# Kernel optimization log

Hardware: AMD Instinct MI355X
Metric: run time of the kernel (lower is better)

The kernel has to match this reference:

```python
import jax, jax.numpy as jnp
import numpy as np

DIM = 192
HEADS = 6
WIN = (8, 7, 7)
SHIFT = (4, 3, 3)


def _rel_pos_index(ws):
    coords = np.stack(np.meshgrid(np.arange(ws[0]), np.arange(ws[1]), np.arange(ws[2]), indexing='ij'))
    cf = coords.reshape(3, -1)
    rc = (cf[:, :, None] - cf[:, None, :]).transpose(1, 2, 0).copy()
    rc[:, :, 0] += ws[0] - 1
    rc[:, :, 1] += ws[1] - 1
    rc[:, :, 2] += ws[2] - 1
    rc[:, :, 0] *= (2 * ws[1] - 1) * (2 * ws[2] - 1)
    rc[:, :, 1] *= 2 * ws[2] - 1
    return rc.sum(-1)  # [N, N]


def _attn_mask(size_dhw, ws, ss):
    # static (shape-only) shift mask, [num_windows, N, N]
    D, H, W = size_dhw
    m = np.zeros(size_dhw, dtype=np.float32)
    sl = [((0, -ws[i]), (-ws[i], -ss[i]), (-ss[i], None)) for i in range(3)]
    cnt = 0
    for d in sl[0]:
        for h in sl[1]:
            for w in sl[2]:
                m[d[0]:d[1], h[0]:h[1], w[0]:w[1]] = cnt
                cnt += 1
    nW = (D // ws[0]) * (H // ws[1]) * (W // ws[2])
    m = m.reshape(D // ws[0], ws[0], H // ws[1], ws[1], W // ws[2], ws[2])
    m = m.transpose(0, 2, 4, 1, 3, 5).reshape(nW, -1)
    diff = m[:, None, :] - m[:, :, None]  # unsqueeze(1) - unsqueeze(2)
    return np.where(diff != 0, np.float32(-100.0), np.float32(0.0))


def setup_inputs() -> dict:
    key = jax.random.key(0)
    ks = jax.random.split(key, 6)
    c = DIM
    x = jax.random.normal(ks[0], (1, 16, 56, 56, c), dtype=jnp.float32)
    qkv_weight = jax.random.normal(ks[1], (3 * c, c), dtype=jnp.float32) * 0.02
    qkv_bias = jax.random.normal(ks[2], (3 * c,), dtype=jnp.float32) * 0.02
    proj_weight = jax.random.normal(ks[3], (c, c), dtype=jnp.float32) * 0.02
    proj_bias = jax.random.normal(ks[4], (c,), dtype=jnp.float32) * 0.02
    tbl = (2 * WIN[0] - 1) * (2 * WIN[1] - 1) * (2 * WIN[2] - 1)
    rel_bias_table = jax.random.normal(ks[5], (tbl, HEADS), dtype=jnp.float32) * 0.02
    return {'x': x, 'qkv_weight': qkv_weight, 'qkv_bias': qkv_bias,
            'proj_weight': proj_weight, 'proj_bias': proj_bias,
            'rel_bias_table': rel_bias_table}


def _forward(x, qkv_weight, qkv_bias, proj_weight, proj_bias, rel_bias_table):
    b, d, h, w, c = x.shape
    ws = list(WIN)
    ss = list(SHIFT)
    for i, s in enumerate((d, h, w)):
        if s <= ws[i]:
            ws[i] = s
            ss[i] = 0
    N = ws[0] * ws[1] * ws[2]
    # relative position bias [1, heads, N, N]
    idx = _rel_pos_index(ws)[:N, :N].reshape(-1)
    rpb = rel_bias_table[idx].reshape(N, N, HEADS).transpose(2, 0, 1)[None]
    # pad to multiples of window
    pad = [(ws[i] - (d, h, w)[i] % ws[i]) % ws[i] for i in range(3)]
    xp = jnp.pad(x, ((0, 0), (0, pad[0]), (0, pad[1]), (0, pad[2]), (0, 0)))
    dp, hp, wp = d + pad[0], h + pad[1], w + pad[2]
    shifted = sum(ss) > 0
    if shifted:
        xp = jnp.roll(xp, shift=(-ss[0], -ss[1], -ss[2]), axis=(1, 2, 3))
    nW = (dp // ws[0]) * (hp // ws[1]) * (wp // ws[2])
    # window partition -> [b*nW, N, c]
    xw = xp.reshape(b, dp // ws[0], ws[0], hp // ws[1], ws[1], wp // ws[2], ws[2], c)
    xw = xw.transpose(0, 1, 3, 5, 2, 4, 6, 7).reshape(b * nW, N, c)
    hd = c // HEADS
    qkv = xw @ qkv_weight.T + qkv_bias
    qkv = qkv.reshape(b * nW, N, 3, HEADS, hd).transpose(2, 0, 3, 1, 4)
    q, k, v = qkv[0], qkv[1], qkv[2]  # [b*nW, heads, N, hd]
    q = q * (hd ** -0.5)
    attn = jnp.einsum('whnd,whmd->whnm', q, k) + rpb
    if shifted:
        mask = jnp.asarray(_attn_mask((dp, hp, wp), ws, ss))  # [nW, N, N]
        attn = attn.reshape(b, nW, HEADS, N, N) + mask[None, :, None]
        attn = attn.reshape(b * nW, HEADS, N, N)
    attn = jax.nn.softmax(attn, axis=-1)
    out = jnp.einsum('whnm,whmd->whnd', attn, v)
    out = out.transpose(0, 2, 1, 3).reshape(b * nW, N, c)
    out = out @ proj_weight.T + proj_bias
    # window reverse
    out = out.reshape(b, dp // ws[0], hp // ws[1], wp // ws[2], ws[0], ws[1], ws[2], c)
    out = out.transpose(0, 1, 4, 2, 5, 3, 6, 7).reshape(b, dp, hp, wp, c)
    if shifted:
        out = jnp.roll(out, shift=(ss[0], ss[1], ss[2]), axis=(1, 2, 3))
    return out[:, :d, :h, :w, :]


def reference(x, qkv_weight, qkv_bias, proj_weight, proj_bias, rel_bias_table):
    return _forward(x, qkv_weight, qkv_bias, proj_weight, proj_bias, rel_bias_table)
```

## Files before the change

kernel.cpp:

```cpp
#include <hip/hip_runtime.h>


typedef _Float16 f16;
typedef __attribute__((ext_vector_type(8))) _Float16 f16x8;
typedef __attribute__((ext_vector_type(4))) _Float16 f16x4;
typedef __attribute__((ext_vector_type(4))) float f32x4;

#define MFMA16(a, b, c) __builtin_amdgcn_mfma_f32_16x16x32_f16((a), (b), (c), 0, 0, 0)

#define HEADS 6
#define NWIN 128
#define NTOK 392
#define TOKENS (NWIN * NTOK)
#define CDIM 192

__device__ inline f16x8 f16x8_zero() {
    f16x8 v = {(f16)0.f,(f16)0.f,(f16)0.f,(f16)0.f,(f16)0.f,(f16)0.f,(f16)0.f,(f16)0.f};
    return v;
}

__global__ __launch_bounds__(256) void wconv_kernel(
    const float* __restrict__ wqkv, const float* __restrict__ wproj,
    f16* __restrict__ wqkv_h, f16* __restrict__ wproj_h)
{
    int i = blockIdx.x * 256 + threadIdx.x;
    if (i < 576 * 192) wqkv_h[i] = (f16)wqkv[i];
    if (i < 192 * 192) wproj_h[i] = (f16)wproj[i];
}

__global__ __launch_bounds__(256) void rpb_kernel(
    const float* __restrict__ tbl, float* __restrict__ rpb)
{
    int i = blockIdx.x * 256 + threadIdx.x;
    if (i >= 6 * 400 * 400) return;
    int h = i / 160000;
    int r = i - h * 160000;
    int n = r / 400;
    int m = r - n * 400;
    float v;
    if (n < NTOK && m < NTOK) {
        int td = n / 49, t2 = n - td * 49, th = t2 / 7, tw = t2 - th * 7;
        int md = m / 49, m2 = m - md * 49, mh = m2 / 7, mw = m2 - mh * 7;
        int idx = ((td - md + 7) * 13 + (th - mh + 6)) * 13 + (tw - mw + 6);
        v = tbl[idx * 6 + h];
    } else {
        v = -1e30f;
    }
    rpb[i] = v;
}

__global__ __launch_bounds__(256, 2) void qkv_kernel(
    const float* __restrict__ x, const f16* __restrict__ wq,
    const float* __restrict__ bq,
    f16* __restrict__ q_ws, f16* __restrict__ k_ws, f16* __restrict__ v_ws)
{
    __shared__ __align__(16) f16 a_lds[64 * 256];
    const int tid = threadIdx.x;
    const int bm = blockIdx.x * 64;
    const int bn = blockIdx.y * 192;

    for (int i = tid; i < 64 * 24; i += 256) {
        int row = i / 24, c = i - row * 24;
        int tok = bm + row;
        int win = tok / NTOK, nloc = tok - win * NTOK;
        int td = nloc / 49, r2 = nloc - td * 49, th = r2 / 7, tw = r2 - th * 7;
        int wd = win >> 6, wh = (win >> 3) & 7, ww = win & 7;
        int d = (wd * 8 + td + 4) & 15;
        int hh = wh * 7 + th + 3; if (hh >= 56) hh -= 56;
        int wco = ww * 7 + tw + 3; if (wco >= 56) wco -= 56;
        const float* src = x + ((d * 56 + hh) * 56 + wco) * CDIM + c * 8;
        const float4 u0 = *(const float4*)(src);
        const float4 u1 = *(const float4*)(src + 4);
        f16x8 v;
        v[0] = (f16)u0.x; v[1] = (f16)u0.y; v[2] = (f16)u0.z; v[3] = (f16)u0.w;
        v[4] = (f16)u1.x; v[5] = (f16)u1.y; v[6] = (f16)u1.z; v[7] = (f16)u1.w;
        *(f16x8*)&a_lds[row * 256 + ((c ^ (row & 7)) << 3)] = v;
    }
    __syncthreads();

    const int lane = tid & 63, wv = tid >> 6;
    const int l15 = lane & 15, g = lane >> 4;
    const int m0 = (wv & 1) * 32, n0 = (wv >> 1) * 96;

    const f32x4 z4 = {0.f, 0.f, 0.f, 0.f};
    f32x4 acc[2][6];
    #pragma unroll
    for (int mi = 0; mi < 2; mi++)
        #pragma unroll
        for (int ni = 0; ni < 6; ni++) acc[mi][ni] = z4;

    #pragma unroll
    for (int kk = 0; kk < 6; kk++) {
        f16x8 af[2];
        #pragma unroll
        for (int mi = 0; mi < 2; mi++) {
            int row = m0 + mi * 16 + l15;
            af[mi] = *(const f16x8*)&a_lds[row * 256 + (((kk * 4 + g) ^ (row & 7)) << 3)];
        }
        #pragma unroll
        for (int ni = 0; ni < 6; ni++) {
            const f16x8 bf = *(const f16x8*)&wq[(bn + n0 + ni * 16 + l15) * CDIM + kk * 32 + g * 8];
            #pragma unroll
            for (int mi = 0; mi < 2; mi++)
                acc[mi][ni] = MFMA16(af[mi], bf, acc[mi][ni]);
        }
    }

    #pragma unroll
    for (int mi = 0; mi < 2; mi++) {
        const int tok0 = bm + m0 + mi * 16 + g * 4;
        const int win = tok0 / NTOK, nloc0 = tok0 - win * NTOK;
        #pragma unroll
        for (int ni = 0; ni < 6; ni++) {
            const int n = bn + n0 + ni * 16 + l15;
            const float bias = bq[n];
            if (bn == 0) {
                const int head = n >> 5, hd = n & 31;
                f16* dst = q_ws + ((win * HEADS + head) * NTOK + nloc0) * 32 + hd;
                #pragma unroll
                for (int j = 0; j < 4; j++)
                    dst[j * 32] = (f16)((acc[mi][ni][j] + bias) * 0.17677669529663687f);
            } else if (bn == 192) {
                const int cc = n - 192, head = cc >> 5, hd = cc & 31;
                f16* dst = k_ws + ((win * HEADS + head) * NTOK + nloc0) * 32 + hd;
                #pragma unroll
                for (int j = 0; j < 4; j++)
                    dst[j * 32] = (f16)(acc[mi][ni][j] + bias);
            } else {
                const int cc = n - 384, head = cc >> 5, hd = cc & 31;
                f16x4 pk;
                #pragma unroll
                for (int j = 0; j < 4; j++) pk[j] = (f16)(acc[mi][ni][j] + bias);
                *(f16x4*)(v_ws + ((win * HEADS + head) * 32 + hd) * NTOK + nloc0) = pk;
            }
        }
    }
}

__global__ __launch_bounds__(256, 2) void attn_kernel(
    const f16* __restrict__ q_ws, const f16* __restrict__ k_ws,
    const f16* __restrict__ v_ws, const float* __restrict__ rpb,
    f16* __restrict__ o_ws)
{
    __shared__ __align__(16) f16 k_lds[25 * 512];
    __shared__ __align__(16) f16 v_lds[13 * 1024];
    __shared__ __align__(16) f16 p_scr[4][512];
    __shared__ unsigned char region[400];

    const int tid = threadIdx.x;
    const int bid = blockIdx.x;
    const int win = bid / 6, head = bid - win * 6;
    const int wd = win >> 6, wh = (win >> 3) & 7, ww = win & 7;
    const f16* kb = k_ws + (win * HEADS + head) * NTOK * 32;
    const f16* vb = v_ws + (win * HEADS + head) * 32 * NTOK;
    const f16* qb = q_ws + (win * HEADS + head) * NTOK * 32;

    for (int i = tid; i < 400; i += 256) {
        unsigned char rr = 0;
        if (i < NTOK) {
            int td = i / 49, r2 = i - td * 49, th = r2 / 7, tw = r2 - th * 7;
            int rd = (wd == 1) ? (td < 4 ? 1 : 2) : 0;
            int rh = (wh == 7) ? (th < 4 ? 1 : 2) : 0;
            int rw = (ww == 7) ? (tw < 4 ? 1 : 2) : 0;
            rr = (unsigned char)(rd * 9 + rh * 3 + rw);
        }
        region[i] = rr;
    }
    for (int i = tid; i < 1600; i += 256) {
        const int tok = ((i >> 6) << 4) | (i & 15);
        const int gg = (i >> 4) & 3;
        f16x8 v = f16x8_zero();
        if (tok < NTOK) v = *(const f16x8*)(kb + tok * 32 + gg * 8);
        *(f16x8*)&k_lds[i * 8] = v;
    }
    for (int i = tid; i < 1664; i += 256) {
        const int tb = i >> 7, rest = i & 127;
        const int hd = ((rest >> 6) << 4) | (rest & 15);
        const int gg = (rest >> 4) & 3;
        const int tok0 = tb * 32 + gg * 8;
        f16x8 v = f16x8_zero();
        if (tok0 < NTOK) v = *(const f16x8*)(vb + hd * NTOK + tok0);
        *(f16x8*)&v_lds[i * 8] = v;
    }
    __syncthreads();

    const int lane = tid & 63, wv = tid >> 6, l15 = lane & 15, g = lane >> 4;
    f16* scr = &p_scr[wv][0];
    const f32x4 z4 = {0.f, 0.f, 0.f, 0.f};

    for (int strip = wv; strip < 25; strip += 4) {
        const int q0 = strip * 16;
        int qr = q0 + l15; if (qr > NTOK - 1) qr = NTOK - 1;
        const f16x8 qf = *(const f16x8*)(qb + qr * 32 + g * 8);

        f32x4 acc[25];
        #pragma unroll
        for (int t = 0; t < 25; t++) {
            const f16x8 kf = *(const f16x8*)&k_lds[t * 512 + lane * 8];
            acc[t] = MFMA16(qf, kf, z4);
        }

        const int rowb = q0 + g * 4;
        unsigned char rrow[4];
        #pragma unroll
        for (int j = 0; j < 4; j++) rrow[j] = region[rowb + j];
        const float* rpbrow = rpb + (head * 400 + rowb) * 400;
        #pragma unroll
        for (int t = 0; t < 25; t++) {
            const int col = t * 16 + l15;
            const unsigned char rc = region[col];
            #pragma unroll
            for (int j = 0; j < 4; j++) {
                const float bias = rpbrow[j * 400 + col];
                acc[t][j] += (rc == rrow[j]) ? bias : (bias - 100.0f);
            }
        }

        float mx[4], rinv[4];
        #pragma unroll
        for (int j = 0; j < 4; j++) {
            float m = acc[0][j];
            #pragma unroll
            for (int t = 1; t < 25; t++) m = fmaxf(m, acc[t][j]);
            m = fmaxf(m, __shfl_xor(m, 1));
            m = fmaxf(m, __shfl_xor(m, 2));
            m = fmaxf(m, __shfl_xor(m, 4));
            m = fmaxf(m, __shfl_xor(m, 8));
            mx[j] = m;
        }
        #pragma unroll
        for (int t = 0; t < 25; t++) {
            #pragma unroll
            for (int j = 0; j < 4; j++) acc[t][j] = __expf(acc[t][j] - mx[j]);
        }
        #pragma unroll
        for (int j = 0; j < 4; j++) {
            float s = 0.f;
            #pragma unroll
            for (int t = 0; t < 25; t++) s += acc[t][j];
            s += __shfl_xor(s, 1);
            s += __shfl_xor(s, 2);
            s += __shfl_xor(s, 4);
            s += __shfl_xor(s, 8);
            rinv[j] = 1.0f / s;
        }

        f32x4 oacc[2] = {z4, z4};
        #pragma unroll
        for (int tb = 0; tb < 13; tb++) {
            #pragma unroll
            for (int half = 0; half < 2; half++) {
                const int t = tb * 2 + half;
                const int tok32 = half * 16 + l15;
                const int wbase = (tok32 >> 3) * 128 + (tok32 & 7);
                #pragma unroll
                for (int j = 0; j < 4; j++) {
                    const f16 pv = (t < 25) ? (f16)acc[t][j] : (f16)0.f;
                    scr[(g * 4 + j) * 8 + wbase] = pv;
                }
            }
            const f16x8 pf = *(const f16x8*)&scr[lane * 8];
            #pragma unroll
            for (int nt = 0; nt < 2; nt++) {
                const f16x8 vf = *(const f16x8*)&v_lds[tb * 1024 + nt * 512 + lane * 8];
                oacc[nt] = MFMA16(pf, vf, oacc[nt]);
            }
        }

        #pragma unroll
        for (int j = 0; j < 4; j++) {
            const int row = rowb + j;
            if (row < NTOK) {
                f16* dst = o_ws + (win * NTOK + row) * CDIM + head * 32;
                dst[l15]      = (f16)(oacc[0][j] * rinv[j]);
                dst[16 + l15] = (f16)(oacc[1][j] * rinv[j]);
            }
        }
    }
}

__global__ __launch_bounds__(256, 2) void proj_kernel(
    const f16* __restrict__ o_ws, const f16* __restrict__ wp,
    const float* __restrict__ bp, float* __restrict__ out)
{
    __shared__ __align__(16) f16 a_lds[64 * 256];
    const int tid = threadIdx.x;
    const int bm = blockIdx.x * 64;
    for (int i = tid; i < 64 * 24; i += 256) {
        int row = i / 24, c = i - row * 24;
        f16x8 v = *(const f16x8*)(o_ws + (bm + row) * CDIM + c * 8);
        *(f16x8*)&a_lds[row * 256 + ((c ^ (row & 7)) << 3)] = v;
    }
    __syncthreads();

    const int lane = tid & 63, wv = tid >> 6;
    const int l15 = lane & 15, g = lane >> 4;
    const int m0 = (wv & 1) * 32, n0 = (wv >> 1) * 96;

    const f32x4 z4 = {0.f, 0.f, 0.f, 0.f};
    f32x4 acc[2][6];
    #pragma unroll
    for (int mi = 0; mi < 2; mi++)
        #pragma unroll
        for (int ni = 0; ni < 6; ni++) acc[mi][ni] = z4;

    #pragma unroll
    for (int kk = 0; kk < 6; kk++) {
        f16x8 af[2];
        #pragma unroll
        for (int mi = 0; mi < 2; mi++) {
            int row = m0 + mi * 16 + l15;
            af[mi] = *(const f16x8*)&a_lds[row * 256 + (((kk * 4 + g) ^ (row & 7)) << 3)];
        }
        #pragma unroll
        for (int ni = 0; ni < 6; ni++) {
            const f16x8 bf = *(const f16x8*)&wp[(n0 + ni * 16 + l15) * CDIM + kk * 32 + g * 8];
            #pragma unroll
            for (int mi = 0; mi < 2; mi++)
                acc[mi][ni] = MFMA16(af[mi], bf, acc[mi][ni]);
        }
    }

    #pragma unroll
    for (int mi = 0; mi < 2; mi++) {
        const int tok0 = bm + m0 + mi * 16 + g * 4;
        #pragma unroll
        for (int j = 0; j < 4; j++) {
            const int tok = tok0 + j;
            const int win = tok / NTOK, nloc = tok - win * NTOK;
            const int td = nloc / 49, r2 = nloc - td * 49, th = r2 / 7, tw = r2 - th * 7;
            const int wd = win >> 6, wh = (win >> 3) & 7, ww = win & 7;
            const int d = (wd * 8 + td + 4) & 15;
            int hh = wh * 7 + th + 3; if (hh >= 56) hh -= 56;
            int wco = ww * 7 + tw + 3; if (wco >= 56) wco -= 56;
            float* dst = out + ((d * 56 + hh) * 56 + wco) * CDIM;
            #pragma unroll
            for (int ni = 0; ni < 6; ni++) {
                const int n = n0 + ni * 16 + l15;
                dst[n] = acc[mi][ni][j] + bp[n];
            }
        }
    }
}

extern "C" void kernel_launch(void* const* d_in, const int* in_sizes, int n_in,
                              void* d_out, int out_size, void* d_ws, size_t ws_size,
                              hipStream_t stream) {
    const float* x     = (const float*)d_in[0];
    const float* wqkv  = (const float*)d_in[1];
    const float* bqkv  = (const float*)d_in[2];
    const float* wproj = (const float*)d_in[3];
    const float* bproj = (const float*)d_in[4];
    const float* rtbl  = (const float*)d_in[5];
    float* out = (float*)d_out;

    const size_t QKV_BYTES = (size_t)NWIN * HEADS * NTOK * 32 * sizeof(f16);
    char* ws = (char*)d_ws;
    f16*   q_ws  = (f16*)(ws);
    f16*   k_ws  = (f16*)(ws + QKV_BYTES);
    f16*   v_ws  = (f16*)(ws + 2 * QKV_BYTES);
    f16*   o_ws  = (f16*)(ws + 3 * QKV_BYTES);
    float* rpb   = (float*)(ws + 4 * QKV_BYTES);
    f16*   wq_h  = (f16*)(ws + 4 * QKV_BYTES + 3840000);
    f16*   wp_h  = (f16*)(ws + 4 * QKV_BYTES + 3840000 + 221184);

    wconv_kernel<<<432, 256, 0, stream>>>(wqkv, wproj, wq_h, wp_h);
    rpb_kernel<<<3750, 256, 0, stream>>>(rtbl, rpb);
    qkv_kernel<<<dim3(784, 3), 256, 0, stream>>>(x, wq_h, bqkv, q_ws, k_ws, v_ws);
    attn_kernel<<<768, 256, 0, stream>>>(q_ws, k_ws, v_ws, rpb, o_ws);
    proj_kernel<<<784, 256, 0, stream>>>(o_ws, wp_h, bproj, out);
}
```

Baseline: 203.1 us.

## Rework attention: transposed QK, exp2 softmax, f16 bias/mask tables, single-pass QKV

Several changes land together. The softmax scale and log2e are folded into the Q weights and bias tables so softmax can use exp2, and relative-position bias and shift masks are precomputed as f16 tables to halve bias traffic. QK^T is computed transposed so each lane holds a full column, which lets P feed a 16x16x16 MFMA directly and drops the LDS scratch round trip. The QKV GEMM now covers all 576 outputs per block so x is gathered once instead of three times. Occupancy hints rise to 3 blocks. Risks include f16 precision on the bias tables and register pressure from the larger accumulator arrays.

```diff
diff --git a/kernel.cpp b/kernel.cpp
--- a/kernel.cpp
+++ b/kernel.cpp
@@ -6,13 +6,16 @@
 typedef __attribute__((ext_vector_type(4))) _Float16 f16x4;
 typedef __attribute__((ext_vector_type(4))) float f32x4;
 
-#define MFMA16(a, b, c) __builtin_amdgcn_mfma_f32_16x16x32_f16((a), (b), (c), 0, 0, 0)
+#define MFMA_K32(a, b, c) __builtin_amdgcn_mfma_f32_16x16x32_f16((a), (b), (c), 0, 0, 0)
+#define MFMA_K16(a, b, c) __builtin_amdgcn_mfma_f32_16x16x16f16((a), (b), (c), 0, 0, 0)
+#define EXP2F(x) __builtin_amdgcn_exp2f(x)
 
 #define HEADS 6
 #define NWIN 128
 #define NTOK 392
-#define TOKENS (NWIN * NTOK)
 #define CDIM 192
+#define LOG2E 1.4426950408889634f
+#define QSCALE 0.2550868562622215f
 
 __device__ inline f16x8 f16x8_zero() {
     f16x8 v = {(f16)0.f,(f16)0.f,(f16)0.f,(f16)0.f,(f16)0.f,(f16)0.f,(f16)0.f,(f16)0.f};
@@ -24,32 +27,49 @@
     f16* __restrict__ wqkv_h, f16* __restrict__ wproj_h)
 {
     int i = blockIdx.x * 256 + threadIdx.x;
-    if (i < 576 * 192) wqkv_h[i] = (f16)wqkv[i];
+    if (i < 576 * 192) {
+        float s = (i < 192 * 192) ? QSCALE : 1.0f;
+        wqkv_h[i] = (f16)(wqkv[i] * s);
+    }
     if (i < 192 * 192) wproj_h[i] = (f16)wproj[i];
 }
 
-__global__ __launch_bounds__(256) void rpb_kernel(
-    const float* __restrict__ tbl, float* __restrict__ rpb)
+__global__ __launch_bounds__(256) void tab_kernel(
+    const float* __restrict__ tbl, f16* __restrict__ rpb_h, f16* __restrict__ mask_h)
 {
     int i = blockIdx.x * 256 + threadIdx.x;
-    if (i >= 6 * 400 * 400) return;
-    int h = i / 160000;
-    int r = i - h * 160000;
-    int n = r / 400;
-    int m = r - n * 400;
-    float v;
-    if (n < NTOK && m < NTOK) {
-        int td = n / 49, t2 = n - td * 49, th = t2 / 7, tw = t2 - th * 7;
-        int md = m / 49, m2 = m - md * 49, mh = m2 / 7, mw = m2 - mh * 7;
-        int idx = ((td - md + 7) * 13 + (th - mh + 6)) * 13 + (tw - mw + 6);
-        v = tbl[idx * 6 + h];
-    } else {
-        v = -1e30f;
-    }
-    rpb[i] = v;
-}
-
-__global__ __launch_bounds__(256, 2) void qkv_kernel(
+    if (i < 6 * 160000) {
+        int h = i / 160000, r = i - h * 160000, n = r / 400, m = r - n * 400;
+        float v;
+        if (n < NTOK && m < NTOK) {
+            int td = n / 49, t2 = n - td * 49, th = t2 / 7, tw = t2 - th * 7;
+            int md = m / 49, m2 = m - md * 49, mh = m2 / 7, mw = m2 - mh * 7;
+            int idx = ((td - md + 7) * 13 + (th - mh + 6)) * 13 + (tw - mw + 6);
+            v = tbl[idx * 6 + h] * LOG2E;
+        } else {
+            v = -60000.0f;
+        }
+        rpb_h[i] = (f16)v;
+    }
+    if (i < 8 * 160000) {
+        int wt = i / 160000, r = i - wt * 160000, n = r / 400, m = r - n * 400;
+        float v = 0.0f;
+        if (n < NTOK && m < NTOK) {
+            int td = n / 49, t2 = n - td * 49, th = t2 / 7, tw = t2 - th * 7;
+            int md = m / 49, m2 = m - md * 49, mh = m2 / 7, mw = m2 - mh * 7;
+            int rn = ((wt & 4) ? (td < 4 ? 1 : 2) : 0) * 9 +
+                     ((wt & 2) ? (th < 4 ? 1 : 2) : 0) * 3 +
+                     ((wt & 1) ? (tw < 4 ? 1 : 2) : 0);
+            int rm = ((wt & 4) ? (md < 4 ? 1 : 2) : 0) * 9 +
+                     ((wt & 2) ? (mh < 4 ? 1 : 2) : 0) * 3 +
+                     ((wt & 1) ? (mw < 4 ? 1 : 2) : 0);
+            v = (rn == rm) ? 0.0f : (-100.0f * LOG2E);
+        }
+        mask_h[i] = (f16)v;
+    }
+}
+
+__global__ __launch_bounds__(256, 3) void qkv_kernel(
     const float* __restrict__ x, const f16* __restrict__ wq,
     const float* __restrict__ bq,
     f16* __restrict__ q_ws, f16* __restrict__ k_ws, f16* __restrict__ v_ws)
@@ -57,7 +77,6 @@
     __shared__ __align__(16) f16 a_lds[64 * 256];
     const int tid = threadIdx.x;
     const int bm = blockIdx.x * 64;
-    const int bn = blockIdx.y * 192;
 
     for (int i = tid; i < 64 * 24; i += 256) {
         int row = i / 24, c = i - row * 24;
@@ -80,92 +99,85 @@
 
     const int lane = tid & 63, wv = tid >> 6;
     const int l15 = lane & 15, g = lane >> 4;
-    const int m0 = (wv & 1) * 32, n0 = (wv >> 1) * 96;
-
+    const int m0 = (wv & 1) * 32, nq = wv >> 1;
     const f32x4 z4 = {0.f, 0.f, 0.f, 0.f};
-    f32x4 acc[2][6];
-    #pragma unroll
-    for (int mi = 0; mi < 2; mi++)
-        #pragma unroll
-        for (int ni = 0; ni < 6; ni++) acc[mi][ni] = z4;
-
-    #pragma unroll
-    for (int kk = 0; kk < 6; kk++) {
-        f16x8 af[2];
+
+    for (int half = 0; half < 2; half++) {
+        const int n0 = half * 288 + nq * 144;
+        f32x4 acc[2][9];
+        #pragma unroll
+        for (int mi = 0; mi < 2; mi++)
+            #pragma unroll
+            for (int ni = 0; ni < 9; ni++) acc[mi][ni] = z4;
+
+        #pragma unroll
+        for (int kk = 0; kk < 6; kk++) {
+            f16x8 af[2];
+            #pragma unroll
+            for (int mi = 0; mi < 2; mi++) {
+                int row = m0 + mi * 16 + l15;
+                af[mi] = *(const f16x8*)&a_lds[row * 256 + (((kk * 4 + g) ^ (row & 7)) << 3)];
+            }
+            #pragma unroll
+            for (int ni = 0; ni < 9; ni++) {
+                const f16x8 bf = *(const f16x8*)&wq[(n0 + ni * 16 + l15) * CDIM + kk * 32 + g * 8];
+                #pragma unroll
+                for (int mi = 0; mi < 2; mi++)
+                    acc[mi][ni] = MFMA_K32(af[mi], bf, acc[mi][ni]);
+            }
+        }
+
         #pragma unroll
         for (int mi = 0; mi < 2; mi++) {
-            int row = m0 + mi * 16 + l15;
-            af[mi] = *(const f16x8*)&a_lds[row * 256 + (((kk * 4 + g) ^ (row & 7)) << 3)];
-        }
-        #pragma unroll
-        for (int ni = 0; ni < 6; ni++) {
-            const f16x8 bf = *(const f16x8*)&wq[(bn + n0 + ni * 16 + l15) * CDIM + kk * 32 + g * 8];
-            #pragma unroll
-            for (int mi = 0; mi < 2; mi++)
-                acc[mi][ni] = MFMA16(af[mi], bf, acc[mi][ni]);
-        }
-    }
-
-    #pragma unroll
-    for (int mi = 0; mi < 2; mi++) {
-        const int tok0 = bm + m0 + mi * 16 + g * 4;
-        const int win = tok0 / NTOK, nloc0 = tok0 - win * NTOK;
-        #pragma unroll
-        for (int ni = 0; ni < 6; ni++) {
-            const int n = bn + n0 + ni * 16 + l15;
-            const float bias = bq[n];
-            if (bn == 0) {
-                const int head = n >> 5, hd = n & 31;
-                f16* dst = q_ws + ((win * HEADS + head) * NTOK + nloc0) * 32 + hd;
-                #pragma unroll
-                for (int j = 0; j < 4; j++)
-                    dst[j * 32] = (f16)((acc[mi][ni][j] + bias) * 0.17677669529663687f);
-            } else if (bn == 192) {
-                const int cc = n - 192, head = cc >> 5, hd = cc & 31;
-                f16* dst = k_ws + ((win * HEADS + head) * NTOK + nloc0) * 32 + hd;
-                #pragma unroll
-                for (int j = 0; j < 4; j++)
-                    dst[j * 32] = (f16)(acc[mi][ni][j] + bias);
-            } else {
-                const int cc = n - 384, head = cc >> 5, hd = cc & 31;
-                f16x4 pk;
-                #pragma unroll
-                for (int j = 0; j < 4; j++) pk[j] = (f16)(acc[mi][ni][j] + bias);
-                *(f16x4*)(v_ws + ((win * HEADS + head) * 32 + hd) * NTOK + nloc0) = pk;
-            }
-        }
-    }
-}
-
-__global__ __launch_bounds__(256, 2) void attn_kernel(
+            const int tok0 = bm + m0 + mi * 16 + g * 4;
+            const int win = tok0 / NTOK, nloc0 = tok0 - win * NTOK;
+            #pragma unroll
+            for (int ni = 0; ni < 9; ni++) {
+                const int n = n0 + ni * 16 + l15;
+                const float bias = bq[n] * ((n < 192) ? QSCALE : 1.0f);
+                if (n < 192) {
+                    const int head = n >> 5, hd = n & 31;
+                    f16* dst = q_ws + ((win * HEADS + head) * NTOK + nloc0) * 32 + hd;
+                    #pragma unroll
+                    for (int j = 0; j < 4; j++)
+                        dst[j * 32] = (f16)(acc[mi][ni][j] + bias);
+                } else if (n < 384) {
+                    const int cc = n - 192, head = cc >> 5, hd = cc & 31;
+                    f16* dst = k_ws + ((win * HEADS + head) * NTOK + nloc0) * 32 + hd;
+                    #pragma unroll
+                    for (int j = 0; j < 4; j++)
+                        dst[j * 32] = (f16)(acc[mi][ni][j] + bias);
+                } else {
+                    const int cc = n - 384, head = cc >> 5, hd = cc & 31;
+                    f16x4 pk;
+                    #pragma unroll
+                    for (int j = 0; j < 4; j++) pk[j] = (f16)(acc[mi][ni][j] + bias);
+                    *(f16x4*)(v_ws + ((win * HEADS + head) * 32 + hd) * NTOK + nloc0) = pk;
+                }
+            }
+        }
+    }
+}
+
+__global__ __launch_bounds__(256, 3) void attn_kernel(
     const f16* __restrict__ q_ws, const f16* __restrict__ k_ws,
-    const f16* __restrict__ v_ws, const float* __restrict__ rpb,
-    f16* __restrict__ o_ws)
+    const f16* __restrict__ v_ws, const f16* __restrict__ rpb_h,
+    const f16* __restrict__ mask_h, f16* __restrict__ o_ws)
 {
     __shared__ __align__(16) f16 k_lds[25 * 512];
-    __shared__ __align__(16) f16 v_lds[13 * 1024];
-    __shared__ __align__(16) f16 p_scr[4][512];
-    __shared__ unsigned char region[400];
+    __shared__ __align__(16) f16 v_lds[32 * 408];
 
     const int tid = threadIdx.x;
     const int bid = blockIdx.x;
     const int win = bid / 6, head = bid - win * 6;
     const int wd = win >> 6, wh = (win >> 3) & 7, ww = win & 7;
-    const f16* kb = k_ws + (win * HEADS + head) * NTOK * 32;
-    const f16* vb = v_ws + (win * HEADS + head) * 32 * NTOK;
-    const f16* qb = q_ws + (win * HEADS + head) * NTOK * 32;
-
-    for (int i = tid; i < 400; i += 256) {
-        unsigned char rr = 0;
-        if (i < NTOK) {
-            int td = i / 49, r2 = i - td * 49, th = r2 / 7, tw = r2 - th * 7;
-            int rd = (wd == 1) ? (td < 4 ? 1 : 2) : 0;
-            int rh = (wh == 7) ? (th < 4 ? 1 : 2) : 0;
-            int rw = (ww == 7) ? (tw < 4 ? 1 : 2) : 0;
-            rr = (unsigned char)(rd * 9 + rh * 3 + rw);
-        }
-        region[i] = rr;
-    }
+    const int wtype = ((wd == 1) ? 4 : 0) | ((wh == 7) ? 2 : 0) | ((ww == 7) ? 1 : 0);
+    const f16* kb = k_ws + (size_t)(win * HEADS + head) * NTOK * 32;
+    const f16* vb = v_ws + (size_t)(win * HEADS + head) * 32 * NTOK;
+    const f16* qb = q_ws + (size_t)(win * HEADS + head) * NTOK * 32;
+    const f16* biasb = rpb_h + head * 160000;
+    const f16* maskb = mask_h + wtype * 160000;
+
     for (int i = tid; i < 1600; i += 256) {
         const int tok = ((i >> 6) << 4) | (i & 15);
         const int gg = (i >> 4) & 3;
@@ -173,19 +185,15 @@
         if (tok < NTOK) v = *(const f16x8*)(kb + tok * 32 + gg * 8);
         *(f16x8*)&k_lds[i * 8] = v;
     }
-    for (int i = tid; i < 1664; i += 256) {
-        const int tb = i >> 7, rest = i & 127;
-        const int hd = ((rest >> 6) << 4) | (rest & 15);
-        const int gg = (rest >> 4) & 3;
-        const int tok0 = tb * 32 + gg * 8;
+    for (int i = tid; i < 32 * 51; i += 256) {
+        const int hd = i / 51, c = i - hd * 51;
         f16x8 v = f16x8_zero();
-        if (tok0 < NTOK) v = *(const f16x8*)(vb + hd * NTOK + tok0);
-        *(f16x8*)&v_lds[i * 8] = v;
+        if (c < 49) v = *(const f16x8*)(vb + hd * NTOK + c * 8);
+        *(f16x8*)&v_lds[hd * 408 + c * 8] = v;
     }
     __syncthreads();
 
     const int lane = tid & 63, wv = tid >> 6, l15 = lane & 15, g = lane >> 4;
-    f16* scr = &p_scr[wv][0];
     const f32x4 z4 = {0.f, 0.f, 0.f, 0.f};
 
     for (int strip = wv; strip < 25; strip += 4) {
@@ -197,89 +205,70 @@
         #pragma unroll
         for (int t = 0; t < 25; t++) {
             const f16x8 kf = *(const f16x8*)&k_lds[t * 512 + lane * 8];
-            acc[t] = MFMA16(qf, kf, z4);
-        }
-
-        const int rowb = q0 + g * 4;
-        unsigned char rrow[4];
-        #pragma unroll
-        for (int j = 0; j < 4; j++) rrow[j] = region[rowb + j];
-        const float* rpbrow = rpb + (head * 400 + rowb) * 400;
-        #pragma unroll
-        for (int t = 0; t < 25; t++) {
-            const int col = t * 16 + l15;
-            const unsigned char rc = region[col];
+            acc[t] = MFMA_K32(kf, qf, z4);
+        }
+
+        const int brow = q0 + l15;
+        const f16* bp = biasb + brow * 400;
+        const f16* mp = maskb + brow * 400;
+        #pragma unroll
+        for (int t = 0; t < 25; t++) {
+            const f16x4 b4 = *(const f16x4*)(bp + t * 16 + g * 4);
+            const f16x4 m4 = *(const f16x4*)(mp + t * 16 + g * 4);
+            #pragma unroll
+            for (int j = 0; j < 4; j++)
+                acc[t][j] += (float)b4[j] + (float)m4[j];
+        }
+
+        float mx = acc[0][0];
+        #pragma unroll
+        for (int t = 0; t < 25; t++) {
+            #pragma unroll
+            for (int j = 0; j < 4; j++) mx = fmaxf(mx, acc[t][j]);
+        }
+        mx = fmaxf(mx, __shfl_xor(mx, 16));
+        mx = fmaxf(mx, __shfl_xor(mx, 32));
+        float s = 0.f;
+        #pragma unroll
+        for (int t = 0; t < 25; t++) {
             #pragma unroll
             for (int j = 0; j < 4; j++) {
-                const float bias = rpbrow[j * 400 + col];
-                acc[t][j] += (rc == rrow[j]) ? bias : (bias - 100.0f);
-            }
-        }
-
-        float mx[4], rinv[4];
+                const float e = EXP2F(acc[t][j] - mx);
+                acc[t][j] = e;
+                s += e;
+            }
+        }
+        s += __shfl_xor(s, 16);
+        s += __shfl_xor(s, 32);
+        const float rinv = 1.0f / s;
+
+        f32x4 oacc[2] = {z4, z4};
+        #pragma unroll
+        for (int t = 0; t < 25; t++) {
+            f16x4 pa;
+            #pragma unroll
+            for (int j = 0; j < 4; j++) pa[j] = (f16)acc[t][j];
+            #pragma unroll
+            for (int nt = 0; nt < 2; nt++) {
+                const f16x4 vf = *(const f16x4*)&v_lds[(nt * 16 + l15) * 408 + t * 16 + g * 4];
+                oacc[nt] = MFMA_K16(pa, vf, oacc[nt]);
+            }
+        }
+
         #pragma unroll
         for (int j = 0; j < 4; j++) {
-            float m = acc[0][j];
-            #pragma unroll
-            for (int t = 1; t < 25; t++) m = fmaxf(m, acc[t][j]);
-            m = fmaxf(m, __shfl_xor(m, 1));
-            m = fmaxf(m, __shfl_xor(m, 2));
-            m = fmaxf(m, __shfl_xor(m, 4));
-            m = fmaxf(m, __shfl_xor(m, 8));
-            mx[j] = m;
-        }
-        #pragma unroll
-        for (int t = 0; t < 25; t++) {
-            #pragma unroll
-            for (int j = 0; j < 4; j++) acc[t][j] = __expf(acc[t][j] - mx[j]);
-        }
-        #pragma unroll
-        for (int j = 0; j < 4; j++) {
-            float s = 0.f;
-            #pragma unroll
-            for (int t = 0; t < 25; t++) s += acc[t][j];
-            s += __shfl_xor(s, 1);
-            s += __shfl_xor(s, 2);
-            s += __shfl_xor(s, 4);
-            s += __shfl_xor(s, 8);
-            rinv[j] = 1.0f / s;
-        }
-
-        f32x4 oacc[2] = {z4, z4};
-        #pragma unroll
-        for (int tb = 0; tb < 13; tb++) {
-            #pragma unroll
-            for (int half = 0; half < 2; half++) {
-                const int t = tb * 2 + half;
-                const int tok32 = half * 16 + l15;
-                const int wbase = (tok32 >> 3) * 128 + (tok32 & 7);
-                #pragma unroll
-                for (int j = 0; j < 4; j++) {
-                    const f16 pv = (t < 25) ? (f16)acc[t][j] : (f16)0.f;
-                    scr[(g * 4 + j) * 8 + wbase] = pv;
-                }
-            }
-            const f16x8 pf = *(const f16x8*)&scr[lane * 8];
-            #pragma unroll
-            for (int nt = 0; nt < 2; nt++) {
-                const f16x8 vf = *(const f16x8*)&v_lds[tb * 1024 + nt * 512 + lane * 8];
-                oacc[nt] = MFMA16(pf, vf, oacc[nt]);
-            }
-        }
-
-        #pragma unroll
-        for (int j = 0; j < 4; j++) {
-            const int row = rowb + j;
+            const float rj = __shfl(rinv, g * 4 + j);
+            const int row = q0 + g * 4 + j;
             if (row < NTOK) {
-                f16* dst = o_ws + (win * NTOK + row) * CDIM + head * 32;
-                dst[l15]      = (f16)(oacc[0][j] * rinv[j]);
-                dst[16 + l15] = (f16)(oacc[1][j] * rinv[j]);
-            }
-        }
-    }
-}
-
-__global__ __launch_bounds__(256, 2) void proj_kernel(
+                f16* dst = o_ws + ((size_t)win * NTOK + row) * CDIM + head * 32;
+                dst[l15]      = (f16)(oacc[0][j] * rj);
+                dst[16 + l15] = (f16)(oacc[1][j] * rj);
+            }
+        }
+    }
+}
+
+__global__ __launch_bounds__(256, 3) void proj_kernel(
     const f16* __restrict__ o_ws, const f16* __restrict__ wp,
     const float* __restrict__ bp, float* __restrict__ out)
 {
@@ -288,7 +277,7 @@
     const int bm = blockIdx.x * 64;
     for (int i = tid; i < 64 * 24; i += 256) {
         int row = i / 24, c = i - row * 24;
-        f16x8 v = *(const f16x8*)(o_ws + (bm + row) * CDIM + c * 8);
+        f16x8 v = *(const f16x8*)(o_ws + (size_t)(bm + row) * CDIM + c * 8);
         *(f16x8*)&a_lds[row * 256 + ((c ^ (row & 7)) << 3)] = v;
     }
     __syncthreads();
@@ -317,7 +306,7 @@
             const f16x8 bf = *(const f16x8*)&wp[(n0 + ni * 16 + l15) * CDIM + kk * 32 + g * 8];
             #pragma unroll
             for (int mi = 0; mi < 2; mi++)
-                acc[mi][ni] = MFMA16(af[mi], bf, acc[mi][ni]);
+                acc[mi][ni] = MFMA_K32(af[mi], bf, acc[mi][ni]);
         }
     }
 
@@ -356,17 +345,18 @@
 
     const size_t QKV_BYTES = (size_t)NWIN * HEADS * NTOK * 32 * sizeof(f16);
     char* ws = (char*)d_ws;
-    f16*   q_ws  = (f16*)(ws);
-    f16*   k_ws  = (f16*)(ws + QKV_BYTES);
-    f16*   v_ws  = (f16*)(ws + 2 * QKV_BYTES);
-    f16*   o_ws  = (f16*)(ws + 3 * QKV_BYTES);
-    float* rpb   = (float*)(ws + 4 * QKV_BYTES);
-    f16*   wq_h  = (f16*)(ws + 4 * QKV_BYTES + 3840000);
-    f16*   wp_h  = (f16*)(ws + 4 * QKV_BYTES + 3840000 + 221184);
+    f16* q_ws   = (f16*)(ws);
+    f16* k_ws   = (f16*)(ws + QKV_BYTES);
+    f16* v_ws   = (f16*)(ws + 2 * QKV_BYTES);
+    f16* o_ws   = (f16*)(ws + 3 * QKV_BYTES);
+    f16* rpb_h  = (f16*)(ws + 4 * QKV_BYTES);
+    f16* mask_h = (f16*)(ws + 4 * QKV_BYTES + 1920000);
+    f16* wq_h   = (f16*)(ws + 4 * QKV_BYTES + 1920000 + 2560000);
+    f16* wp_h   = (f16*)(ws + 4 * QKV_BYTES + 1920000 + 2560000 + 221184);
 
     wconv_kernel<<<432, 256, 0, stream>>>(wqkv, wproj, wq_h, wp_h);
-    rpb_kernel<<<3750, 256, 0, stream>>>(rtbl, rpb);
-    qkv_kernel<<<dim3(784, 3), 256, 0, stream>>>(x, wq_h, bqkv, q_ws, k_ws, v_ws);
-    attn_kernel<<<768, 256, 0, stream>>>(q_ws, k_ws, v_ws, rpb, o_ws);
+    tab_kernel<<<5000, 256, 0, stream>>>(rtbl, rpb_h, mask_h);
+    qkv_kernel<<<784, 256, 0, stream>>>(x, wq_h, bqkv, q_ws, k_ws, v_ws);
+    attn_kernel<<<768, 256, 0, stream>>>(q_ws, k_ws, v_ws, rpb_h, mask_h, o_ws);
     proj_kernel<<<784, 256, 0, stream>>>(o_ws, wp_h, bproj, out);
 }
```

Measured after the change: 373.5 us. 83.9% more time.
